# Kernel optimization log

Measured on AMD Instinct MI355X. Metric: run time of the kernel, lower is better.

Reference implementation:

```python
import jax, jax.numpy as jnp
import numpy as np

B, S, D, H = 8, 1024, 768, 12
HEAD_DIM = D // H  # 64
# NOTE: original code divides scores by scaling=(head_dim)**-0.5, i.e. MULTIPLIES by sqrt(head_dim)
SCORE_SCALE = float(HEAD_DIM) ** 0.5


def setup_inputs() -> dict:
    key = jax.random.key(0)
    ks = jax.random.split(key, 9)
    std = 1.0 / np.sqrt(D)
    return {
        "x":  jax.random.normal(ks[0], (B, S, D), jnp.float32),
        "Wq": jax.random.normal(ks[1], (H, D, D), jnp.float32) * std,
        "bq": jax.random.normal(ks[2], (H, D), jnp.float32) * std,
        "Wk": jax.random.normal(ks[3], (H, D, D), jnp.float32) * std,
        "bk": jax.random.normal(ks[4], (H, D), jnp.float32) * std,
        "Wv": jax.random.normal(ks[5], (H, D, D), jnp.float32) * std,
        "bv": jax.random.normal(ks[6], (H, D), jnp.float32) * std,
        "Wp": jax.random.normal(ks[7], (H * D, D), jnp.float32) * (1.0 / np.sqrt(H * D)),
        "bp": jax.random.normal(ks[8], (D,), jnp.float32) * std,
    }


def reference(x, Wq, bq, Wk, bk, Wv, bv, Wp, bp):
    # Per-head full-width projections, batched over the head axis h.
    q = jnp.einsum('bsd,hde->bhse', x, Wq) + bq[None, :, None, :]  # [B,H,S,D]
    k = jnp.einsum('bsd,hde->bhse', x, Wk) + bk[None, :, None, :]
    v = jnp.einsum('bsd,hde->bhse', x, Wv) + bv[None, :, None, :]
    scores = jnp.einsum('bhse,bhte->bhst', q, k) * SCORE_SCALE    # [B,H,S,S]
    attn = jax.nn.softmax(scores, axis=-1)
    o = jnp.einsum('bhst,bhte->bhse', attn, v)                     # [B,H,S,D]
    # concat heads along last dim (head-major order matches torch.cat)
    o = jnp.transpose(o, (0, 2, 1, 3)).reshape(B, S, H * D)        # [B,S,H*D]
    return o @ Wp + bp                                             # [B,S,D]
```

## Files before the change

kernel.cpp:

```cpp
#include <hip/hip_runtime.h>


typedef __attribute__((ext_vector_type(8))) short bf16x8;
typedef __attribute__((ext_vector_type(4))) float fx4;

#define NB 8
#define NS 1024
#define ND 768
#define NH 12

__device__ __forceinline__ unsigned short f2bf(float x) {
    unsigned int u = __float_as_uint(x);
    u += 0x7fffu + ((u >> 16) & 1u);
    return (unsigned short)(u >> 16);
}
__device__ __forceinline__ float bf2f(unsigned short h) {
    return __uint_as_float(((unsigned int)h) << 16);
}

__device__ __forceinline__ void gll16(const void* g, void* l) {
    __builtin_amdgcn_global_load_lds(
        (const __attribute__((address_space(1))) void*)g,
        (__attribute__((address_space(3))) void*)l, 16, 0, 0);
}

__device__ __forceinline__ void split_body(const float* __restrict__ in,
                                           unsigned short* __restrict__ hi,
                                           unsigned short* __restrict__ lo, int i) {
    float4 v = ((const float4*)in)[i];
    ushort4 h, l;
    h.x = f2bf(v.x); l.x = f2bf(v.x - bf2f(h.x));
    h.y = f2bf(v.y); l.y = f2bf(v.y - bf2f(h.y));
    h.z = f2bf(v.z); l.z = f2bf(v.z - bf2f(h.z));
    h.w = f2bf(v.w); l.w = f2bf(v.w - bf2f(h.w));
    ((ushort4*)hi)[i] = h;
    ((ushort4*)lo)[i] = l;
}

template<int NTERMS, class Epi>
__device__ __forceinline__ void gemm_core(
    char* __restrict__ smem,
    const unsigned short* __restrict__ Ah, const unsigned short* __restrict__ Al, int lda,
    const unsigned short* __restrict__ Bh, const unsigned short* __restrict__ Bl, int ldb,
    int K, Epi epi)
{
    const int t = threadIdx.x;
    const int lane = t & 63;
    const int w = t >> 6;
    const int wm = (w >> 1) << 6;
    const int wn = (w & 1) << 6;
    const int lr = lane & 15;
    const int lg = lane >> 4;

    const int srA = (w << 5) + (lane >> 2);
    const int swz = (srA >> 1) & 3;
    const int skb = (((lane & 3) ^ swz) << 4);
    const int ldso = w << 11;

    const long ga0 = (long)srA * lda * 2 + skb;
    const long ga1 = ga0 + (long)lda * 32;
    const long gb0 = (long)srA * ldb * 2 + skb;
    const long gb1 = gb0 + (long)ldb * 32;

    const char* pAh = (const char*)Ah;
    const char* pBh = (const char*)Bh;
    const char* pAl = (const char*)Al;
    const char* pBl = (const char*)Bl;
    char* smA  = smem;
    char* smB  = smem + 8192;
    char* smA2 = smem + ((NTERMS == 3) ? 16384 : 0);
    char* smB2 = smem + ((NTERMS == 3) ? 24576 : 8192);

    int offA[4], offB[4];
    #pragma unroll
    for (int i = 0; i < 4; i++) {
        int ra = wm + (i << 4) + lr;
        offA[i] = ra * 32 + ((lg ^ ((ra >> 1) & 3)) << 3);
        int rb = wn + (i << 4) + lr;
        offB[i] = rb * 32 + ((lg ^ ((rb >> 1) & 3)) << 3);
    }

    fx4 acc[4][4] = {};

    for (int k0 = 0; k0 < K; k0 += 32) {
        const long kb2 = (long)k0 * 2;
        __syncthreads();
        gll16(pAh + ga0 + kb2, smA + ldso);
        gll16(pAh + ga1 + kb2, smA + ldso + 1024);
        gll16(pBh + gb0 + kb2, smB + ldso);
        gll16(pBh + gb1 + kb2, smB + ldso + 1024);
        if constexpr (NTERMS == 3) {
            gll16(pAl + ga0 + kb2, smA2 + ldso);
            gll16(pAl + ga1 + kb2, smA2 + ldso + 1024);
            gll16(pBl + gb0 + kb2, smB2 + ldso);
            gll16(pBl + gb1 + kb2, smB2 + ldso + 1024);
        }
        __syncthreads();

        bf16x8 fa[4], fb[4], fa2[4], fb2[4];
        #pragma unroll
        for (int i = 0; i < 4; i++) {
            fa[i] = *(const bf16x8*)((const unsigned short*)smA + offA[i]);
            fb[i] = *(const bf16x8*)((const unsigned short*)smB + offB[i]);
        }
        if constexpr (NTERMS == 3) {
            #pragma unroll
            for (int i = 0; i < 4; i++) {
                fa2[i] = *(const bf16x8*)((const unsigned short*)smA2 + offA[i]);
                fb2[i] = *(const bf16x8*)((const unsigned short*)smB2 + offB[i]);
            }
        }
        #pragma unroll
        for (int i = 0; i < 4; i++)
            #pragma unroll
            for (int j = 0; j < 4; j++) {
                acc[i][j] = __builtin_amdgcn_mfma_f32_16x16x32_bf16(fa[i], fb[j], acc[i][j], 0, 0, 0);
                if constexpr (NTERMS == 3) {
                    acc[i][j] = __builtin_amdgcn_mfma_f32_16x16x32_bf16(fa[i], fb2[j], acc[i][j], 0, 0, 0);
                    acc[i][j] = __builtin_amdgcn_mfma_f32_16x16x32_bf16(fa2[i], fb[j], acc[i][j], 0, 0, 0);
                }
            }
    }

    #pragma unroll
    for (int i = 0; i < 4; i++)
        #pragma unroll
        for (int j = 0; j < 4; j++)
            #pragma unroll
            for (int r = 0; r < 4; r++)
                epi(wm + (i << 4) + (lg << 2) + r, wn + (j << 4) + lr, acc[i][j][r]);
}

__device__ __forceinline__ void softmax_rows(float* __restrict__ Sc, int blk) {
    int row = blk * 4 + ((int)threadIdx.x >> 6);
    int lane = threadIdx.x & 63;
    float* rp = Sc + (long)row * NS;
    const float4* src = (const float4*)rp + (lane << 2);
    float v[16];
    #pragma unroll
    for (int i = 0; i < 4; i++) {
        float4 a = src[i];
        v[i * 4 + 0] = a.x; v[i * 4 + 1] = a.y; v[i * 4 + 2] = a.z; v[i * 4 + 3] = a.w;
    }
    float m = v[0];
    #pragma unroll
    for (int i = 1; i < 16; i++) m = fmaxf(m, v[i]);
    #pragma unroll
    for (int o = 32; o > 0; o >>= 1) m = fmaxf(m, __shfl_xor(m, o));
    float s = 0.f, p[16];
    #pragma unroll
    for (int i = 0; i < 16; i++) { p[i] = __expf((v[i] - m) * 8.0f); s += p[i]; }
    #pragma unroll
    for (int o = 32; o > 0; o >>= 1) s += __shfl_xor(s, o);
    float inv = 1.0f / s;
    unsigned int wrd[8];
    #pragma unroll
    for (int i = 0; i < 8; i++) {
        unsigned int u0 = f2bf(p[2 * i] * inv);
        unsigned int u1 = f2bf(p[2 * i + 1] * inv);
        wrd[i] = u0 | (u1 << 16);
    }
    uint4* dst = (uint4*)((unsigned short*)rp + (lane << 4));
    dst[0] = make_uint4(wrd[0], wrd[1], wrd[2], wrd[3]);
    dst[1] = make_uint4(wrd[4], wrd[5], wrd[6], wrd[7]);
}

__global__ void k_setup1(
    const float* __restrict__ x, unsigned short* __restrict__ xh, unsigned short* __restrict__ xl,
    const float* __restrict__ Wq, unsigned short* __restrict__ Wqh, unsigned short* __restrict__ Wql,
    const float* __restrict__ Wk, unsigned short* __restrict__ Wkh, unsigned short* __restrict__ Wkl,
    const float* __restrict__ bq, float* __restrict__ rk)
{
    const int bx = blockIdx.x;
    if (bx < 6144) {
        split_body(x, xh, xl, bx * 256 + threadIdx.x);
    } else if (bx < 13056) {
        split_body(Wq, Wqh, Wql, (bx - 6144) * 256 + threadIdx.x);
    } else if (bx < 19968) {
        split_body(Wk, Wkh, Wkl, (bx - 13056) * 256 + threadIdx.x);
    } else {
        const int idx = bx - 19968;
        const int h = idx / 192;
        const int d = (idx % 192) * 4 + ((int)threadIdx.x >> 6);
        const int lane = threadIdx.x & 63;
        const float4* row = (const float4*)(Wk + ((long)h * ND + d) * ND);
        const float4* bv4 = (const float4*)(bq + h * ND);
        float acc = 0.f;
        #pragma unroll
        for (int i = 0; i < 3; i++) {
            float4 a = row[lane + (i << 6)];
            float4 b = bv4[lane + (i << 6)];
            acc += a.x * b.x + a.y * b.y + a.z * b.z + a.w * b.w;
        }
        #pragma unroll
        for (int o = 32; o > 0; o >>= 1) acc += __shfl_xor(acc, o);
        if (lane == 0) rk[h * ND + d] = acc;
    }
}

__global__ __launch_bounds__(256, 2) void k_setup2(
    const unsigned short* __restrict__ Wkh, const unsigned short* __restrict__ Wkl,
    const unsigned short* __restrict__ Wqh, const unsigned short* __restrict__ Wql,
    unsigned short* __restrict__ MTh, unsigned short* __restrict__ MTl,
    const float* __restrict__ x, const float* __restrict__ rk, float* __restrict__ w_all)
{
    __shared__ __align__(16) char smem[36864];
    const int bx = blockIdx.x;
    if (bx < 432) {
        const int n0 = (bx % 6) << 7;
        const int m0 = ((bx / 6) % 6) << 7;
        const long hw = (long)(bx / 36) * (ND * ND);
        unsigned short* oh = MTh + hw + (long)m0 * ND + n0;
        unsigned short* ol = MTl + hw + (long)m0 * ND + n0;
        gemm_core<3>(smem, Wkh + hw + (long)m0 * ND, Wkl + hw + (long)m0 * ND, ND,
                     Wqh + hw + (long)n0 * ND, Wql + hw + (long)n0 * ND, ND, ND,
                     [=](int r, int c, float v) {
                         unsigned short hh = f2bf(v);
                         oh[r * ND + c] = hh;
                         ol[r * ND + c] = f2bf(v - bf2f(hh));
                     });
    } else {
        float* srk = (float*)smem;
        for (int i = threadIdx.x; i < NH * ND; i += 256) srk[i] = rk[i];
        __syncthreads();
        const int row = (bx - 432) * 4 + ((int)threadIdx.x >> 6);
        const int lane = threadIdx.x & 63;
        const float4* xr = (const float4*)(x + (long)row * ND);
        float4 xa[3];
        #pragma unroll
        for (int i = 0; i < 3; i++) xa[i] = xr[lane + (i << 6)];
        for (int h = 0; h < NH; h++) {
            const float* r = srk + h * ND;
            float acc = 0.f;
            #pragma unroll
            for (int i = 0; i < 3; i++) {
                int e = (lane + (i << 6)) << 2;
                acc += xa[i].x * r[e] + xa[i].y * r[e + 1]
                     + xa[i].z * r[e + 2] + xa[i].w * r[e + 3];
            }
            #pragma unroll
            for (int o = 32; o > 0; o >>= 1) acc += __shfl_xor(acc, o);
            if (lane == 0) w_all[h * (NB * NS) + row] = acc;
        }
    }
}

__global__ void k_setup3(const float* __restrict__ Wv, unsigned short* __restrict__ Wvb,
                         const float* __restrict__ Wp, unsigned short* __restrict__ WpT)
{
    __shared__ float tile[64][65];
    const int bx = blockIdx.x;
    if (bx < 6912) {
        int i = bx * 256 + threadIdx.x;
        float4 v = ((const float4*)Wv)[i];
        ushort4 h;
        h.x = f2bf(v.x); h.y = f2bf(v.y); h.z = f2bf(v.z); h.w = f2bf(v.w);
        ((ushort4*)Wvb)[i] = h;
    } else {
        const int idx = bx - 6912;
        const int c0 = (idx % 12) * 64;
        const int r0 = ((idx / 12) % 12) * 64;
        const long zo = (long)(idx / 144) * (ND * ND);
        const float* in = Wp + zo;
        unsigned short* oh = WpT + zo;
        const int tc = threadIdx.x & 63, t4 = threadIdx.x >> 6;
        #pragma unroll
        for (int i = 0; i < 16; i++) {
            int r = (i << 2) + t4;
            tile[r][tc] = in[(long)(r0 + r) * ND + c0 + tc];
        }
        __syncthreads();
        #pragma unroll
        for (int i = 0; i < 16; i++) {
            int c = (i << 2) + t4;
            oh[(long)(c0 + c) * ND + r0 + tc] = f2bf(tile[tc][c]);
        }
    }
}

__global__ __launch_bounds__(256, 2) void k_setup4(
    const unsigned short* __restrict__ WpT, const unsigned short* __restrict__ Wvb,
    unsigned short* __restrict__ NTo, const float* __restrict__ bv,
    float* __restrict__ s_all)
{
    __shared__ __align__(16) char smem[16384];
    const int bx = blockIdx.x;
    if (bx < 432) {
        const int n0 = (bx % 6) << 7;
        const int m0 = ((bx / 6) % 6) << 7;
        const long hw = (long)(bx / 36) * (ND * ND);
        unsigned short* o = NTo + hw + (long)m0 * ND + n0;
        gemm_core<1>(smem, WpT + hw + (long)m0 * ND, nullptr, ND,
                     Wvb + hw + (long)n0 * ND, nullptr, ND, ND,
                     [=](int r, int c, float v) { o[r * ND + c] = f2bf(v); });
    } else {
        const int idx = bx - 432;
        const int h = idx / 192;
        const int j = (idx % 192) * 4 + ((int)threadIdx.x >> 6);
        const int lane = threadIdx.x & 63;
        const ushort4* row = (const ushort4*)(WpT + ((long)h * ND + j) * ND);
        const float* bvh = bv + h * ND;
        float acc = 0.f;
        #pragma unroll
        for (int i = 0; i < 3; i++) {
            int c = lane + (i << 6);
            ushort4 u = row[c];
            int e = c << 2;
            acc += bf2f(u.x) * bvh[e] + bf2f(u.y) * bvh[e + 1]
                 + bf2f(u.z) * bvh[e + 2] + bf2f(u.w) * bvh[e + 3];
        }
        #pragma unroll
        for (int o = 32; o > 0; o >>= 1) acc += __shfl_xor(acc, o);
        if (lane == 0) s_all[h * ND + j] = acc;
    }
}


__global__ __launch_bounds__(256, 2) void k_G0(
    const unsigned short* __restrict__ xh, const unsigned short* __restrict__ xl,
    const unsigned short* __restrict__ MTh, const unsigned short* __restrict__ MTl,
    unsigned short* __restrict__ Gh, unsigned short* __restrict__ Gl)
{
    __shared__ __align__(16) char smem[32768];
    const int bx = blockIdx.x;
    const int xcd = bx & 7, idx = bx >> 3;
    const int m0 = (xcd * 8 + idx / 6) << 7;
    const int n0 = (idx % 6) << 7;
    unsigned short* oh = Gh + (long)m0 * ND + n0;
    unsigned short* ol = Gl + (long)m0 * ND + n0;
    gemm_core<3>(smem, xh + (long)m0 * ND, xl + (long)m0 * ND, ND,
                 MTh + (long)n0 * ND, MTl + (long)n0 * ND, ND, ND,
                 [=](int r, int c, float v) {
                     unsigned short hh = f2bf(v);
                     oh[(long)r * ND + c] = hh;
                     ol[(long)r * ND + c] = f2bf(v - bf2f(hh));
                 });
}

__global__ __launch_bounds__(256, 2) void k_scores(
    const unsigned short* __restrict__ Gh, const unsigned short* __restrict__ Gl,
    const unsigned short* __restrict__ xh, const unsigned short* __restrict__ xl,
    const float* __restrict__ wv, float* __restrict__ Sc)
{
    __shared__ __align__(16) char smem[32768];
    const int bx = blockIdx.x;
    const int bl = bx & 7, idx = bx >> 3;
    const int m0 = (idx >> 3) << 7;
    const int n0 = (idx & 7) << 7;
    const long ao = ((long)bl * NS + m0) * ND;
    const long bo = ((long)bl * NS + n0) * ND;
    const float* ww = wv + bl * NS + n0;
    float* out = Sc + ((long)bl * NS + m0) * NS + n0;
    gemm_core<3>(smem, Gh + ao, Gl + ao, ND, xh + bo, xl + bo, ND, ND,
                 [=](int r, int c, float v) { out[(long)r * NS + c] = v + ww[c]; });
}

__global__ __launch_bounds__(256, 2) void k_ZSM(
    const unsigned short* __restrict__ xh, const unsigned short* __restrict__ NTh,
    const float* __restrict__ sh, unsigned short* __restrict__ ZT,
    float* __restrict__ Sc)
{
    __shared__ __align__(16) char smem[16384];
    const int bx = blockIdx.x;
    if (bx < 384) {
        const int xcd = bx & 7, idx = bx >> 3;
        const int m0 = (xcd * 8 + idx / 6) << 7;
        const int n0 = (idx % 6) << 7;
        const int bl = m0 >> 10;
        const int s0 = m0 & (NS - 1);
        unsigned short* zt = ZT + (long)bl * (ND * NS);
        gemm_core<1>(smem, xh + (long)m0 * ND, nullptr, ND,
                     NTh + (long)n0 * ND, nullptr, ND, ND,
                     [=](int r, int c, float v) {
                         zt[(long)(n0 + c) * NS + s0 + r] = f2bf(v + sh[n0 + c]);
                     });
    } else {
        softmax_rows(Sc, bx - 384);
    }
}

template<int MODE>
__global__ __launch_bounds__(256, 2) void k_PVG(
    const unsigned short* __restrict__ P, const unsigned short* __restrict__ ZT,
    const float* __restrict__ bp, float* __restrict__ outp,
    const unsigned short* __restrict__ xh, const unsigned short* __restrict__ xl,
    const unsigned short* __restrict__ MTh, const unsigned short* __restrict__ MTl,
    unsigned short* __restrict__ Gh, unsigned short* __restrict__ Gl)
{
    __shared__ __align__(16) char smem[32768];
    const int bx = blockIdx.x;
    if (bx < 384) {
        const int bl = bx & 7, idx = bx >> 3;
        const int m0 = (idx / 6) << 7;
        const int n0 = (idx % 6) << 7;
        const unsigned short* A = P + ((long)bl * NS + m0) * (2 * NS);
        const unsigned short* B = ZT + (long)bl * (ND * NS) + (long)n0 * NS;
        float* o = outp + ((long)bl * NS + m0) * ND + n0;
        const float* bi = bp + n0;
        gemm_core<1>(smem, A, nullptr, 2 * NS, B, nullptr, NS, NS,
                     [=](int r, int c, float v) {
                         float* d = o + (long)r * ND + c;
                         if constexpr (MODE == 0) *d = v + bi[c];
                         else *d += v;
                     });
    } else {
        const int g = bx - 384;
        const int xcd = g & 7, idx = g >> 3;
        const int m0 = (xcd * 8 + idx / 6) << 7;
        const int n0 = (idx % 6) << 7;
        unsigned short* oh = Gh + (long)m0 * ND + n0;
        unsigned short* ol = Gl + (long)m0 * ND + n0;
        gemm_core<3>(smem, xh + (long)m0 * ND, xl + (long)m0 * ND, ND,
                     MTh + (long)n0 * ND, MTl + (long)n0 * ND, ND, ND,
                     [=](int r, int c, float v) {
                         unsigned short hh = f2bf(v);
                         oh[(long)r * ND + c] = hh;
                         ol[(long)r * ND + c] = f2bf(v - bf2f(hh));
                     });
    }
}


extern "C" void kernel_launch(void* const* d_in, const int* in_sizes, int n_in,
                              void* d_out, int out_size, void* d_ws, size_t ws_size,
                              hipStream_t stream) {
    (void)in_sizes; (void)n_in; (void)out_size; (void)ws_size;
    const float* x  = (const float*)d_in[0];
    const float* Wq = (const float*)d_in[1];
    const float* bq = (const float*)d_in[2];
    const float* Wk = (const float*)d_in[3];
    const float* bk = (const float*)d_in[4];  (void)bk;
    const float* Wv = (const float*)d_in[5];
    const float* bv = (const float*)d_in[6];
    const float* Wp = (const float*)d_in[7];
    const float* bp = (const float*)d_in[8];

    const size_t nx  = (size_t)NB * NS * ND;
    const size_t nw  = (size_t)NH * ND * ND;

    char* p = (char*)d_ws;
    auto alloc = [&](size_t bytes) -> void* {
        void* r = (void*)p;
        p += (bytes + 255) & ~(size_t)255;
        return r;
    };
    unsigned short* xh   = (unsigned short*)alloc(nx * 2);
    unsigned short* xl   = (unsigned short*)alloc(nx * 2);
    unsigned short* MTh  = (unsigned short*)alloc(nw * 2);
    unsigned short* MTl  = (unsigned short*)alloc(nw * 2);
    unsigned short* NTb  = (unsigned short*)alloc(nw * 2);
    float*          rk   = (float*)alloc((size_t)NH * ND * 4);
    float*          s_all= (float*)alloc((size_t)NH * ND * 4);
    float*          w_all= (float*)alloc((size_t)NH * NB * NS * 4);
    char* U = (char*)alloc(2 * nx * 2 + ((size_t)NB * NS * NS * 4) + ((size_t)NB * NS * ND * 2));
    unsigned short* Wqh = (unsigned short*)U;
    unsigned short* Wql = Wqh + nw;
    unsigned short* Wkh = Wql + nw;
    unsigned short* Wkl = Wkh + nw;
    unsigned short* Wvb = (unsigned short*)U;
    unsigned short* WpT = Wvb + nw;
    unsigned short* Gh = (unsigned short*)U;
    unsigned short* Gl = Gh + nx;
    float*          Sc = (float*)(Gl + nx);
    unsigned short* ZT = (unsigned short*)(Sc + (size_t)NB * NS * NS);

    k_setup1<<<22272, 256, 0, stream>>>(x, xh, xl, Wq, Wqh, Wql, Wk, Wkh, Wkl, bq, rk);
    k_setup2<<<2480, 256, 0, stream>>>(Wkh, Wkl, Wqh, Wql, MTh, MTl, x, rk, w_all);
    k_setup3<<<8640, 256, 0, stream>>>(Wv, Wvb, Wp, WpT);
    k_setup4<<<2736, 256, 0, stream>>>(WpT, Wvb, NTb, bv, s_all);

    k_G0<<<384, 256, 0, stream>>>(xh, xl, MTh, MTl, Gh, Gl);
    for (int h = 0; h < NH; h++) {
        const long hwn = (long)(h + 1) * ND * ND;
        k_scores<<<512, 256, 0, stream>>>(Gh, Gl, xh, xl,
                                          w_all + (long)h * NB * NS, Sc);
        k_ZSM<<<2432, 256, 0, stream>>>(xh, NTb + (long)h * ND * ND,
                                        s_all + h * ND, ZT, Sc);
        const int ng = (h + 1 < NH) ? 768 : 384;
        if (h == 0)
            k_PVG<0><<<ng, 256, 0, stream>>>((unsigned short*)Sc, ZT, bp, (float*)d_out,
                                             xh, xl, MTh + hwn, MTl + hwn, Gh, Gl);
        else
            k_PVG<1><<<ng, 256, 0, stream>>>((unsigned short*)Sc, ZT, bp, (float*)d_out,
                                             xh, xl,
                                             MTh + ((h + 1 < NH) ? hwn : 0),
                                             MTl + ((h + 1 < NH) ? hwn : 0), Gh, Gl);
    }
}
```

Baseline: 1.494 ms.

## Double GEMM K-step to 64 with new LDS swizzle and regroup per-head kernels

The shared GEMM core now stages 64-wide K slices per iteration, with a new XOR swizzle over 8 chunks. This halves the number of barrier pairs per tile but doubles LDS use, up to 64KB for the 3-term kernels, which may limit occupancy. The per-head scores GEMM and the Z-projection GEMM are merged into one launch. Softmax moves into its own kernel after them instead of sharing a launch with the Z GEMM. Setup GEMM blocks are also remapped so that each XCD gets a contiguous range of tiles.

```diff
diff --git a/kernel.cpp b/kernel.cpp
--- a/kernel.cpp
+++ b/kernel.cpp
@@ -44,6 +44,8 @@
     const unsigned short* __restrict__ Bh, const unsigned short* __restrict__ Bl, int ldb,
     int K, Epi epi)
 {
+    constexpr int TILE = 16384;
+
     const int t = threadIdx.x;
     const int lane = t & 63;
     const int w = t >> 6;
@@ -52,74 +54,76 @@
     const int lr = lane & 15;
     const int lg = lane >> 4;
 
-    const int srA = (w << 5) + (lane >> 2);
-    const int swz = (srA >> 1) & 3;
-    const int skb = (((lane & 3) ^ swz) << 4);
-    const int ldso = w << 11;
-
-    const long ga0 = (long)srA * lda * 2 + skb;
-    const long ga1 = ga0 + (long)lda * 32;
-    const long gb0 = (long)srA * ldb * 2 + skb;
-    const long gb1 = gb0 + (long)ldb * 32;
+    const int l3 = lane >> 3;
+    const int cs = (lane & 7) ^ l3;
+    const int ldsw = w << 12;
+
+    const long gsA = (long)(w * 32 + l3) * lda * 2 + cs * 16;
+    const long gsB = (long)(w * 32 + l3) * ldb * 2 + cs * 16;
+    const long giA = (long)lda * 16;
+    const long giB = (long)ldb * 16;
 
     const char* pAh = (const char*)Ah;
     const char* pBh = (const char*)Bh;
     const char* pAl = (const char*)Al;
     const char* pBl = (const char*)Bl;
     char* smA  = smem;
-    char* smB  = smem + 8192;
-    char* smA2 = smem + ((NTERMS == 3) ? 16384 : 0);
-    char* smB2 = smem + ((NTERMS == 3) ? 24576 : 8192);
-
-    int offA[4], offB[4];
+    char* smB  = smem + TILE;
+    char* smA2 = smem + ((NTERMS == 3) ? 2 * TILE : 0);
+    char* smB2 = smem + ((NTERMS == 3) ? 3 * TILE : TILE);
+
+    int rowA[4], rowB[4];
     #pragma unroll
     for (int i = 0; i < 4; i++) {
-        int ra = wm + (i << 4) + lr;
-        offA[i] = ra * 32 + ((lg ^ ((ra >> 1) & 3)) << 3);
-        int rb = wn + (i << 4) + lr;
-        offB[i] = rb * 32 + ((lg ^ ((rb >> 1) & 3)) << 3);
-    }
+        rowA[i] = (wm + (i << 4) + lr) << 6;
+        rowB[i] = (wn + (i << 4) + lr) << 6;
+    }
+    const int lr7 = lr & 7;
 
     fx4 acc[4][4] = {};
 
-    for (int k0 = 0; k0 < K; k0 += 32) {
+    for (int k0 = 0; k0 < K; k0 += 64) {
         const long kb2 = (long)k0 * 2;
         __syncthreads();
-        gll16(pAh + ga0 + kb2, smA + ldso);
-        gll16(pAh + ga1 + kb2, smA + ldso + 1024);
-        gll16(pBh + gb0 + kb2, smB + ldso);
-        gll16(pBh + gb1 + kb2, smB + ldso + 1024);
-        if constexpr (NTERMS == 3) {
-            gll16(pAl + ga0 + kb2, smA2 + ldso);
-            gll16(pAl + ga1 + kb2, smA2 + ldso + 1024);
-            gll16(pBl + gb0 + kb2, smB2 + ldso);
-            gll16(pBl + gb1 + kb2, smB2 + ldso + 1024);
+        #pragma unroll
+        for (int ii = 0; ii < 4; ii++) {
+            const int lo = ldsw + (ii << 10);
+            gll16(pAh + gsA + ii * giA + kb2, smA + lo);
+            gll16(pBh + gsB + ii * giB + kb2, smB + lo);
+            if constexpr (NTERMS == 3) {
+                gll16(pAl + gsA + ii * giA + kb2, smA2 + lo);
+                gll16(pBl + gsB + ii * giB + kb2, smB2 + lo);
+            }
         }
         __syncthreads();
 
-        bf16x8 fa[4], fb[4], fa2[4], fb2[4];
-        #pragma unroll
-        for (int i = 0; i < 4; i++) {
-            fa[i] = *(const bf16x8*)((const unsigned short*)smA + offA[i]);
-            fb[i] = *(const bf16x8*)((const unsigned short*)smB + offB[i]);
-        }
-        if constexpr (NTERMS == 3) {
+        #pragma unroll
+        for (int kk = 0; kk < 2; kk++) {
+            const int pc = (((kk << 2) + lg) ^ lr7) << 3;
+            bf16x8 fa[4], fb[4], fa2[4], fb2[4];
             #pragma unroll
             for (int i = 0; i < 4; i++) {
-                fa2[i] = *(const bf16x8*)((const unsigned short*)smA2 + offA[i]);
-                fb2[i] = *(const bf16x8*)((const unsigned short*)smB2 + offB[i]);
+                fa[i] = *(const bf16x8*)((const unsigned short*)smA + rowA[i] + pc);
+                fb[i] = *(const bf16x8*)((const unsigned short*)smB + rowB[i] + pc);
             }
-        }
-        #pragma unroll
-        for (int i = 0; i < 4; i++)
-            #pragma unroll
-            for (int j = 0; j < 4; j++) {
-                acc[i][j] = __builtin_amdgcn_mfma_f32_16x16x32_bf16(fa[i], fb[j], acc[i][j], 0, 0, 0);
-                if constexpr (NTERMS == 3) {
-                    acc[i][j] = __builtin_amdgcn_mfma_f32_16x16x32_bf16(fa[i], fb2[j], acc[i][j], 0, 0, 0);
-                    acc[i][j] = __builtin_amdgcn_mfma_f32_16x16x32_bf16(fa2[i], fb[j], acc[i][j], 0, 0, 0);
+            if constexpr (NTERMS == 3) {
+                #pragma unroll
+                for (int i = 0; i < 4; i++) {
+                    fa2[i] = *(const bf16x8*)((const unsigned short*)smA2 + rowA[i] + pc);
+                    fb2[i] = *(const bf16x8*)((const unsigned short*)smB2 + rowB[i] + pc);
                 }
             }
+            #pragma unroll
+            for (int i = 0; i < 4; i++)
+                #pragma unroll
+                for (int j = 0; j < 4; j++) {
+                    acc[i][j] = __builtin_amdgcn_mfma_f32_16x16x32_bf16(fa[i], fb[j], acc[i][j], 0, 0, 0);
+                    if constexpr (NTERMS == 3) {
+                        acc[i][j] = __builtin_amdgcn_mfma_f32_16x16x32_bf16(fa[i], fb2[j], acc[i][j], 0, 0, 0);
+                        acc[i][j] = __builtin_amdgcn_mfma_f32_16x16x32_bf16(fa2[i], fb[j], acc[i][j], 0, 0, 0);
+                    }
+                }
+        }
     }
 
     #pragma unroll
@@ -204,12 +208,13 @@
     unsigned short* __restrict__ MTh, unsigned short* __restrict__ MTl,
     const float* __restrict__ x, const float* __restrict__ rk, float* __restrict__ w_all)
 {
-    __shared__ __align__(16) char smem[36864];
+    __shared__ __align__(16) char smem[65536];
     const int bx = blockIdx.x;
     if (bx < 432) {
-        const int n0 = (bx % 6) << 7;
-        const int m0 = ((bx / 6) % 6) << 7;
-        const long hw = (long)(bx / 36) * (ND * ND);
+        const int tid = (bx & 7) * 54 + (bx >> 3);
+        const int n0 = (tid % 6) << 7;
+        const int m0 = ((tid / 6) % 6) << 7;
+        const long hw = (long)(tid / 36) * (ND * ND);
         unsigned short* oh = MTh + hw + (long)m0 * ND + n0;
         unsigned short* ol = MTl + hw + (long)m0 * ND + n0;
         gemm_core<3>(smem, Wkh + hw + (long)m0 * ND, Wkl + hw + (long)m0 * ND, ND,
@@ -283,12 +288,13 @@
     unsigned short* __restrict__ NTo, const float* __restrict__ bv,
     float* __restrict__ s_all)
 {
-    __shared__ __align__(16) char smem[16384];
+    __shared__ __align__(16) char smem[32768];
     const int bx = blockIdx.x;
     if (bx < 432) {
-        const int n0 = (bx % 6) << 7;
-        const int m0 = ((bx / 6) % 6) << 7;
-        const long hw = (long)(bx / 36) * (ND * ND);
+        const int tid = (bx & 7) * 54 + (bx >> 3);
+        const int n0 = (tid % 6) << 7;
+        const int m0 = ((tid / 6) % 6) << 7;
+        const long hw = (long)(tid / 36) * (ND * ND);
         unsigned short* o = NTo + hw + (long)m0 * ND + n0;
         gemm_core<1>(smem, WpT + hw + (long)m0 * ND, nullptr, ND,
                      Wvb + hw + (long)n0 * ND, nullptr, ND, ND,
@@ -321,7 +327,7 @@
     const unsigned short* __restrict__ MTh, const unsigned short* __restrict__ MTl,
     unsigned short* __restrict__ Gh, unsigned short* __restrict__ Gl)
 {
-    __shared__ __align__(16) char smem[32768];
+    __shared__ __align__(16) char smem[65536];
     const int bx = blockIdx.x;
     const int xcd = bx & 7, idx = bx >> 3;
     const int m0 = (xcd * 8 + idx / 6) << 7;
@@ -337,33 +343,28 @@
                  });
 }
 
-__global__ __launch_bounds__(256, 2) void k_scores(
+__global__ __launch_bounds__(256, 2) void k_SZ(
     const unsigned short* __restrict__ Gh, const unsigned short* __restrict__ Gl,
     const unsigned short* __restrict__ xh, const unsigned short* __restrict__ xl,
-    const float* __restrict__ wv, float* __restrict__ Sc)
-{
-    __shared__ __align__(16) char smem[32768];
-    const int bx = blockIdx.x;
-    const int bl = bx & 7, idx = bx >> 3;
-    const int m0 = (idx >> 3) << 7;
-    const int n0 = (idx & 7) << 7;
-    const long ao = ((long)bl * NS + m0) * ND;
-    const long bo = ((long)bl * NS + n0) * ND;
-    const float* ww = wv + bl * NS + n0;
-    float* out = Sc + ((long)bl * NS + m0) * NS + n0;
-    gemm_core<3>(smem, Gh + ao, Gl + ao, ND, xh + bo, xl + bo, ND, ND,
-                 [=](int r, int c, float v) { out[(long)r * NS + c] = v + ww[c]; });
-}
-
-__global__ __launch_bounds__(256, 2) void k_ZSM(
-    const unsigned short* __restrict__ xh, const unsigned short* __restrict__ NTh,
-    const float* __restrict__ sh, unsigned short* __restrict__ ZT,
-    float* __restrict__ Sc)
-{
-    __shared__ __align__(16) char smem[16384];
-    const int bx = blockIdx.x;
-    if (bx < 384) {
-        const int xcd = bx & 7, idx = bx >> 3;
+    const float* __restrict__ wv, float* __restrict__ Sc,
+    const unsigned short* __restrict__ NTh, const float* __restrict__ sh,
+    unsigned short* __restrict__ ZT)
+{
+    __shared__ __align__(16) char smem[65536];
+    const int bx = blockIdx.x;
+    if (bx < 512) {
+        const int bl = bx & 7, idx = bx >> 3;
+        const int m0 = (idx >> 3) << 7;
+        const int n0 = (idx & 7) << 7;
+        const long ao = ((long)bl * NS + m0) * ND;
+        const long bo = ((long)bl * NS + n0) * ND;
+        const float* ww = wv + bl * NS + n0;
+        float* out = Sc + ((long)bl * NS + m0) * NS + n0;
+        gemm_core<3>(smem, Gh + ao, Gl + ao, ND, xh + bo, xl + bo, ND, ND,
+                     [=](int r, int c, float v) { out[(long)r * NS + c] = v + ww[c]; });
+    } else {
+        const int g = bx - 512;
+        const int xcd = g & 7, idx = g >> 3;
         const int m0 = (xcd * 8 + idx / 6) << 7;
         const int n0 = (idx % 6) << 7;
         const int bl = m0 >> 10;
@@ -374,9 +375,11 @@
                      [=](int r, int c, float v) {
                          zt[(long)(n0 + c) * NS + s0 + r] = f2bf(v + sh[n0 + c]);
                      });
-    } else {
-        softmax_rows(Sc, bx - 384);
-    }
+    }
+}
+
+__global__ __launch_bounds__(256) void k_SM(float* __restrict__ Sc) {
+    softmax_rows(Sc, blockIdx.x);
 }
 
 template<int MODE>
@@ -387,7 +390,7 @@
     const unsigned short* __restrict__ MTh, const unsigned short* __restrict__ MTl,
     unsigned short* __restrict__ Gh, unsigned short* __restrict__ Gl)
 {
-    __shared__ __align__(16) char smem[32768];
+    __shared__ __align__(16) char smem[65536];
     const int bx = blockIdx.x;
     if (bx < 384) {
         const int bl = bx & 7, idx = bx >> 3;
@@ -472,10 +475,9 @@
     k_G0<<<384, 256, 0, stream>>>(xh, xl, MTh, MTl, Gh, Gl);
     for (int h = 0; h < NH; h++) {
         const long hwn = (long)(h + 1) * ND * ND;
-        k_scores<<<512, 256, 0, stream>>>(Gh, Gl, xh, xl,
-                                          w_all + (long)h * NB * NS, Sc);
-        k_ZSM<<<2432, 256, 0, stream>>>(xh, NTb + (long)h * ND * ND,
-                                        s_all + h * ND, ZT, Sc);
+        k_SZ<<<896, 256, 0, stream>>>(Gh, Gl, xh, xl, w_all + (long)h * NB * NS,
+                                      Sc, NTb + (long)h * ND * ND, s_all + h * ND, ZT);
+        k_SM<<<2048, 256, 0, stream>>>(Sc);
         const int ng = (h + 1 < NH) ? 768 : 384;
         if (h == 0)
             k_PVG<0><<<ng, 256, 0, stream>>>((unsigned short*)Sc, ZT, bp, (float*)d_out,
```

New measurement: 1.381 ms. 1.08x faster.
